# Kernel optimization log

Hardware: AMD Instinct MI355X
Metric: run time of the kernel (lower is better)

## Reference

```python
import jax, jax.numpy as jnp
import numpy as np

INF = 100000.0
B, W, T, U, S, N = 64, 16, 64, 128, 20, 8


def setup_inputs() -> dict:
    key = jax.random.key(0)
    ks = jax.random.split(key, 9)
    xavier = (2.0 / (U + U)) ** 0.5
    return {
        "slot_utt_h": jax.random.normal(ks[0], (B, W, T, U), jnp.float32),
        "slot_candidate_c": jax.random.normal(ks[1], (S, U), jnp.float32),
        "status_candidate_c": jax.random.normal(ks[2], (N, U), jnp.float32),
        "position_encoding": jax.random.normal(ks[3], (B, W, S, U), jnp.float32),
        "q_status": jax.random.normal(ks[4], (B, W, N, U), jnp.float32),
        "mask": jnp.zeros((B, W, S * N), jnp.float32),
        "weight": jax.random.normal(ks[5], (U, U), jnp.float32) * xavier,  # bilinear co-attention weight [U,U]
        "W1": jax.random.normal(ks[6], (2 * U, U), jnp.float32) * 0.05,
        "b1": jnp.zeros((U,), jnp.float32),
        "W2": jax.random.normal(ks[7], (U, U), jnp.float32) * 0.05,
        "b2": jnp.zeros((U,), jnp.float32),
        "W3": jax.random.normal(ks[8], (U, 1), jnp.float32) * 0.05,
        "b3": jnp.zeros((1,), jnp.float32),
    }


def _zero_mask(p):
    # original: -(p == 0).float() * INF, added before softmax
    return jnp.where(p == 0.0, -INF, 0.0)


def reference(slot_utt_h, slot_candidate_c, status_candidate_c, position_encoding,
              q_status, mask, weight, W1, b1, W2, b2, W3, b3):
    # ---- attention over utterance tokens ----
    # p[b,w,s,t] = <slot_candidate_c[s], slot_utt_h[b,w,t]>
    p = jnp.einsum('su,bwtu->bwst', slot_candidate_c, slot_utt_h)
    p = jax.nn.softmax(p + _zero_mask(p), axis=-1)
    q_slot = jnp.einsum('bwst,bwtu->bwsu', p, slot_utt_h) + position_encoding  # [B,W,S,U]

    # ---- bilinear co-attention: [B,W*S,U] @ weight @ [B,U,W*N] -> [B,W,S,W,N] ----
    co = jnp.einsum('bwsu,uv,bxnv->bwsxn', q_slot, weight, q_status)
    p2 = jax.nn.softmax(co + _zero_mask(co), axis=3)  # softmax over the second window axis x

    # weighted sum of statuses over window axis x
    q_status_slot = jnp.einsum('bwsxn,bxnu->bwsnu', p2, q_status)  # [B,W,S,N,U]

    q_slot_exp = jnp.broadcast_to(q_slot[:, :, :, None, :], (B, W, S, N, U))
    features = jnp.concatenate([q_slot_exp, q_status_slot], axis=-1)  # [B,W,S,N,2U]

    # ---- MLP (dropout in eval mode = identity) ----
    h = jax.nn.relu(features @ W1 + b1)
    h = jax.nn.relu(h @ W2 + b2)
    logits = h @ W3 + b3  # [B,W,S,N,1]

    logits = logits.reshape(B, W, S * N)
    slot_pred_logits = jnp.max(logits + mask, axis=1)  # masked max-pool over window
    slot_pred_labels = (slot_pred_logits > 0.0).astype(jnp.float32)
    return (slot_pred_labels, S * N, slot_pred_logits)
```

## Files before the change

### kernel.cpp

```cpp
#include <hip/hip_runtime.h>
#include <math.h>

#define INF_ 100000.0f
constexpr int B_ = 64, W_ = 16, T_ = 64, U_ = 128, S_ = 20, N_ = 8;

typedef unsigned short ushort_t;
typedef __attribute__((ext_vector_type(8))) short bf16x8;
typedef __attribute__((ext_vector_type(4))) float floatx4;

static __device__ __forceinline__ unsigned short f2bf(float x) {
    unsigned int u = __float_as_uint(x);
    return (unsigned short)((u + 0x7fff + ((u >> 16) & 1)) >> 16);
}
static __device__ __forceinline__ float bf2f(unsigned short s) {
    return __uint_as_float(((unsigned int)s) << 16);
}

__global__ __launch_bounds__(256) void k0_cast(
    const float* __restrict__ q_status, const float* __restrict__ weight,
    const float* __restrict__ W1, const float* __restrict__ W2,
    ushort_t* __restrict__ qstat_bf, ushort_t* __restrict__ wcomb,
    ushort_t* __restrict__ w1botT, ushort_t* __restrict__ w2T)
{
    int idx = blockIdx.x * 256 + threadIdx.x;
    if (idx < 1048576) { qstat_bf[idx] = f2bf(q_status[idx]); return; }
    idx -= 1048576;
    if (idx < 32768) {
        int j = idx >> 7, k = idx & 127;
        float v = (j < 128) ? weight[k * 128 + j] : W1[k * 128 + (j - 128)];
        wcomb[idx] = f2bf(v); return;
    }
    idx -= 32768;
    if (idx < 16384) {
        int j = idx >> 7, k = idx & 127;
        w1botT[idx] = f2bf(W1[(128 + k) * 128 + j]); return;
    }
    idx -= 16384;
    if (idx < 16384) {
        int j = idx >> 7, k = idx & 127;
        w2T[idx] = f2bf(W2[k * 128 + j]); return;
    }
}

__global__ __launch_bounds__(256) void k1_attn(
    const float* __restrict__ h,
    const float* __restrict__ c,
    const float* __restrict__ pos,
    ushort_t* __restrict__ q_slot_bf)
{
    __shared__ __align__(16) ushort_t sh_h[64 * 136];
    __shared__ __align__(16) ushort_t sh_hT[128 * 72];
    __shared__ __align__(16) ushort_t sh_c[32 * 136];
    __shared__ __align__(16) float    sh_sc[32 * 68];
    __shared__ __align__(16) ushort_t sh_P[32 * 72];

    const int bw = blockIdx.x, tid = threadIdx.x;
    const float* hb = h + (size_t)bw * 8192;
    for (int i = tid; i < 8192; i += 256) {
        int t = i >> 7, u = i & 127;
        ushort_t v = f2bf(hb[i]);
        sh_h[t * 136 + u] = v;
        sh_hT[u * 72 + t] = v;
    }
    for (int i = tid; i < 4096; i += 256) {
        int s = i >> 7;
        sh_c[s * 136 + (i & 127)] = (s < 20) ? f2bf(c[i]) : (ushort_t)0;
    }
    for (int i = tid; i < 32 * 72; i += 256) sh_P[i] = 0;
    __syncthreads();

    const int wave = tid >> 6, lane = tid & 63, m16 = lane & 15, q = lane >> 4;

#pragma unroll
    for (int ci = 0; ci < 2; ++ci) {
        int cmb = wave * 2 + ci;
        int mt = cmb >> 2, jt = cmb & 3;
        floatx4 acc = {0.f, 0.f, 0.f, 0.f};
#pragma unroll
        for (int kt = 0; kt < 4; ++kt) {
            bf16x8 a = *(const bf16x8*)&sh_c[(mt * 16 + m16) * 136 + kt * 32 + q * 8];
            bf16x8 b = *(const bf16x8*)&sh_h[(jt * 16 + m16) * 136 + kt * 32 + q * 8];
            acc = __builtin_amdgcn_mfma_f32_16x16x32_bf16(a, b, acc, 0, 0, 0);
        }
#pragma unroll
        for (int reg = 0; reg < 4; ++reg)
            sh_sc[(mt * 16 + q * 4 + reg) * 68 + jt * 16 + m16] = acc[reg];
    }
    __syncthreads();

    for (int s = wave; s < 20; s += 4) {
        float v = sh_sc[s * 68 + lane];
        if (v == 0.0f) v = -INF_;
        float m = v;
        for (int d = 32; d; d >>= 1) m = fmaxf(m, __shfl_xor(m, d));
        float e = expf(v - m);
        float sum = e;
        for (int d = 32; d; d >>= 1) sum += __shfl_xor(sum, d);
        sh_P[s * 72 + lane] = f2bf(e / sum);
    }
    __syncthreads();

    const size_t obase = (size_t)bw * 2560;
#pragma unroll
    for (int ci = 0; ci < 4; ++ci) {
        int cmb = wave * 4 + ci;
        int mt = cmb >> 3, jt = cmb & 7;
        floatx4 acc = {0.f, 0.f, 0.f, 0.f};
#pragma unroll
        for (int kt = 0; kt < 2; ++kt) {
            bf16x8 a = *(const bf16x8*)&sh_P[(mt * 16 + m16) * 72 + kt * 32 + q * 8];
            bf16x8 b = *(const bf16x8*)&sh_hT[(jt * 16 + m16) * 72 + kt * 32 + q * 8];
            acc = __builtin_amdgcn_mfma_f32_16x16x32_bf16(a, b, acc, 0, 0, 0);
        }
        int u = jt * 16 + m16;
#pragma unroll
        for (int reg = 0; reg < 4; ++reg) {
            int row = mt * 16 + q * 4 + reg;
            if (row < 20)
                q_slot_bf[obase + row * 128 + u] =
                    f2bf(acc[reg] + pos[obase + row * 128 + u]);
        }
    }
}

__global__ __launch_bounds__(256) void k2a(
    const ushort_t* __restrict__ qs_bf,
    const ushort_t* __restrict__ wcomb,
    const float* __restrict__ b1,
    ushort_t* __restrict__ qw_bf,
    float* __restrict__ A)
{
    __shared__ __align__(16) ushort_t sh_w[256 * 136];
    const int tid = threadIdx.x;
    for (int i = tid * 4; i < 32768; i += 1024) {
        int j = i >> 7, k = i & 127;
        *(ushort4*)&sh_w[j * 136 + k] = *(const ushort4*)&wcomb[i];
    }
    __syncthreads();

    const int wave = tid >> 6, lane = tid & 63, m16 = lane & 15, q = lane >> 4;
    const size_t row = (size_t)blockIdx.x * 64 + wave * 16 + m16;

    floatx4 acc[16];
#pragma unroll
    for (int jt = 0; jt < 16; ++jt) acc[jt] = (floatx4){0.f, 0.f, 0.f, 0.f};

#pragma unroll
    for (int kt = 0; kt < 4; ++kt) {
        bf16x8 a = *(const bf16x8*)&qs_bf[row * 128 + kt * 32 + q * 8];
#pragma unroll
        for (int jt = 0; jt < 16; ++jt) {
            bf16x8 b = *(const bf16x8*)&sh_w[(jt * 16 + m16) * 136 + kt * 32 + q * 8];
            acc[jt] = __builtin_amdgcn_mfma_f32_16x16x32_bf16(a, b, acc[jt], 0, 0, 0);
        }
    }

    const size_t orow0 = (size_t)blockIdx.x * 64 + wave * 16 + q * 4;
#pragma unroll
    for (int jt = 0; jt < 16; ++jt) {
        int col = jt * 16 + m16;
        if (col < 128) {
#pragma unroll
            for (int reg = 0; reg < 4; ++reg)
                qw_bf[(orow0 + reg) * 128 + col] = f2bf(acc[jt][reg]);
        } else {
            float bv = b1[col - 128];
#pragma unroll
            for (int reg = 0; reg < 4; ++reg)
                A[(orow0 + reg) * 128 + (col - 128)] = acc[jt][reg] + bv;
        }
    }
}

__global__ __launch_bounds__(256) void k2b(
    const ushort_t* __restrict__ qstat_bf,
    const ushort_t* __restrict__ w1botT,
    ushort_t* __restrict__ qs1_bf)
{
    __shared__ __align__(16) ushort_t sh_w[128 * 136];
    const int tid = threadIdx.x;
    for (int i = tid * 4; i < 16384; i += 1024) {
        int j = i >> 7, k = i & 127;
        *(ushort4*)&sh_w[j * 136 + k] = *(const ushort4*)&w1botT[i];
    }
    __syncthreads();

    const int wave = tid >> 6, lane = tid & 63, m16 = lane & 15, q = lane >> 4;
    const size_t row = (size_t)blockIdx.x * 64 + wave * 16 + m16;

    floatx4 acc[8];
#pragma unroll
    for (int jt = 0; jt < 8; ++jt) acc[jt] = (floatx4){0.f, 0.f, 0.f, 0.f};
#pragma unroll
    for (int kt = 0; kt < 4; ++kt) {
        bf16x8 a = *(const bf16x8*)&qstat_bf[row * 128 + kt * 32 + q * 8];
#pragma unroll
        for (int jt = 0; jt < 8; ++jt) {
            bf16x8 b = *(const bf16x8*)&sh_w[(jt * 16 + m16) * 136 + kt * 32 + q * 8];
            acc[jt] = __builtin_amdgcn_mfma_f32_16x16x32_bf16(a, b, acc[jt], 0, 0, 0);
        }
    }
    const size_t orow0 = (size_t)blockIdx.x * 64 + wave * 16 + q * 4;
#pragma unroll
    for (int jt = 0; jt < 8; ++jt) {
        int col = jt * 16 + m16;
#pragma unroll
        for (int reg = 0; reg < 4; ++reg)
            qs1_bf[(orow0 + reg) * 128 + col] = f2bf(acc[jt][reg]);
    }
}

__global__ __launch_bounds__(256) void k3_co(
    const ushort_t* __restrict__ qw_bf,
    const ushort_t* __restrict__ qstat_bf,
    float* __restrict__ co)
{
    __shared__ __align__(16) ushort_t sh_y[128 * 136];
    const int tid = threadIdx.x, rt = blockIdx.x, b = blockIdx.y;
    for (int i = tid * 4; i < 16384; i += 1024) {
        int j = i >> 7, k = i & 127;
        *(ushort4*)&sh_y[j * 136 + k] = *(const ushort4*)&qstat_bf[(size_t)b * 16384 + i];
    }
    __syncthreads();

    const int wave = tid >> 6, lane = tid & 63, m16 = lane & 15, q = lane >> 4;
    const size_t rbase = (size_t)b * 320 + rt * 64 + wave * 16;

    floatx4 acc[8];
#pragma unroll
    for (int jt = 0; jt < 8; ++jt) acc[jt] = (floatx4){0.f, 0.f, 0.f, 0.f};
#pragma unroll
    for (int kt = 0; kt < 4; ++kt) {
        bf16x8 a = *(const bf16x8*)&qw_bf[(rbase + m16) * 128 + kt * 32 + q * 8];
#pragma unroll
        for (int jt = 0; jt < 8; ++jt) {
            bf16x8 b2_ = *(const bf16x8*)&sh_y[(jt * 16 + m16) * 136 + kt * 32 + q * 8];
            acc[jt] = __builtin_amdgcn_mfma_f32_16x16x32_bf16(a, b2_, acc[jt], 0, 0, 0);
        }
    }
#pragma unroll
    for (int jt = 0; jt < 8; ++jt)
#pragma unroll
        for (int reg = 0; reg < 4; ++reg)
            co[(rbase + q * 4 + reg) * 128 + jt * 16 + m16] = acc[jt][reg];
}

__global__ __launch_bounds__(640, 3) void k4_fused(
    const float* __restrict__ co,
    const ushort_t* __restrict__ qs1_bf,
    const float* __restrict__ A,
    const ushort_t* __restrict__ w2T,
    const float* __restrict__ b2,
    const float* __restrict__ W3,
    const float* __restrict__ b3,
    float* __restrict__ lg)
{
    __shared__ __align__(16) ushort_t sh_qs1[128 * 136];
    __shared__ __align__(16) ushort_t sh_w2t[128 * 136];
    __shared__ __align__(16) float sh_p2[20 * 128];

    const int bw = blockIdx.x, b = bw >> 4, tid = threadIdx.x;

    for (int i = tid * 4; i < 16384; i += 2560) {
        int r = i >> 7, k = i & 127;
        *(ushort4*)&sh_qs1[r * 136 + k] = *(const ushort4*)&qs1_bf[(size_t)b * 16384 + i];
        *(ushort4*)&sh_w2t[r * 136 + k] = *(const ushort4*)&w2T[i];
    }

    if (tid < 160) {
        int s = tid >> 3, n = tid & 7;
        const float* crow = co + ((size_t)bw * 20 + s) * 128;
        float v[16];
        float m = -INFINITY;
#pragma unroll
        for (int x = 0; x < 16; ++x) {
            float t = crow[x * 8 + n];
            if (t == 0.0f) t = -INF_;
            v[x] = t;
            m = fmaxf(m, t);
        }
        float sum = 0.f;
#pragma unroll
        for (int x = 0; x < 16; ++x) { v[x] = expf(v[x] - m); sum += v[x]; }
        float r = 1.0f / sum;
#pragma unroll
        for (int x = 0; x < 16; ++x) sh_p2[s * 128 + x * 8 + n] = v[x] * r;
    }
    __syncthreads();

    const int wave = tid >> 6, lane = tid & 63, m16 = lane & 15, q = lane >> 4;
    const int row = wave * 16 + m16;
    const int s = row >> 3, n = row & 7;

    floatx4 acc[8];
#pragma unroll
    for (int jt = 0; jt < 8; ++jt) acc[jt] = (floatx4){0.f, 0.f, 0.f, 0.f};

    const float* Ab = A + (size_t)bw * 20 * 128;

#pragma unroll
    for (int kt = 0; kt < 4; ++kt) {
        const int k0 = kt * 32 + q * 8;
        bf16x8 bfr[8];
#pragma unroll
        for (int jt = 0; jt < 8; ++jt)
            bfr[jt] = *(const bf16x8*)&sh_w2t[(jt * 16 + m16) * 136 + k0];

        float hv[8];
        const float* ar = Ab + s * 128 + k0;
        float4 a0 = *(const float4*)ar;
        float4 a1 = *(const float4*)(ar + 4);
        hv[0] = a0.x; hv[1] = a0.y; hv[2] = a0.z; hv[3] = a0.w;
        hv[4] = a1.x; hv[5] = a1.y; hv[6] = a1.z; hv[7] = a1.w;
#pragma unroll
        for (int x = 0; x < 16; ++x) {
            float p = sh_p2[s * 128 + x * 8 + n];
            bf16x8 qv = *(const bf16x8*)&sh_qs1[(x * 8 + n) * 136 + k0];
            hv[0] += p * bf2f((ushort_t)qv[0]);
            hv[1] += p * bf2f((ushort_t)qv[1]);
            hv[2] += p * bf2f((ushort_t)qv[2]);
            hv[3] += p * bf2f((ushort_t)qv[3]);
            hv[4] += p * bf2f((ushort_t)qv[4]);
            hv[5] += p * bf2f((ushort_t)qv[5]);
            hv[6] += p * bf2f((ushort_t)qv[6]);
            hv[7] += p * bf2f((ushort_t)qv[7]);
        }
        bf16x8 af;
#pragma unroll
        for (int e = 0; e < 8; ++e) af[e] = (short)f2bf(fmaxf(hv[e], 0.f));
#pragma unroll
        for (int jt = 0; jt < 8; ++jt)
            acc[jt] = __builtin_amdgcn_mfma_f32_16x16x32_bf16(
                af, bfr[jt], acc[jt], 0, 0, 0);
    }

    float b2v[8], w3v[8];
#pragma unroll
    for (int jt = 0; jt < 8; ++jt) {
        b2v[jt] = b2[jt * 16 + m16];
        w3v[jt] = W3[jt * 16 + m16];
    }
    const float b3v = b3[0];

#pragma unroll
    for (int reg = 0; reg < 4; ++reg) {
        float p = 0.f;
#pragma unroll
        for (int jt = 0; jt < 8; ++jt)
            p += fmaxf(acc[jt][reg] + b2v[jt], 0.f) * w3v[jt];
        p += __shfl_xor(p, 1);
        p += __shfl_xor(p, 2);
        p += __shfl_xor(p, 4);
        p += __shfl_xor(p, 8);
        if (m16 == 0)
            lg[(size_t)bw * 160 + wave * 16 + q * 4 + reg] = p + b3v;
    }
}

__global__ __launch_bounds__(256) void k5_final(
    const float* __restrict__ lg,
    const float* __restrict__ mask,
    float* __restrict__ out)
{
    int idx = blockIdx.x * 256 + threadIdx.x;
    const int SN = S_ * N_;
    if (idx < B_ * SN) {
        int b = idx / SN, sn = idx % SN;
        float m = -INFINITY;
        for (int w = 0; w < W_; ++w) {
            float v = lg[((size_t)b * W_ + w) * SN + sn] + mask[((size_t)b * W_ + w) * SN + sn];
            m = fmaxf(m, v);
        }
        out[idx] = (m > 0.f) ? 1.f : 0.f;
        out[B_ * SN + 1 + idx] = m;
    }
    if (idx == 0) out[B_ * SN] = (float)SN;
}

extern "C" void kernel_launch(void* const* d_in, const int* in_sizes, int n_in,
                              void* d_out, int out_size, void* d_ws, size_t ws_size,
                              hipStream_t stream) {
    const float* slot_utt_h = (const float*)d_in[0];
    const float* slot_candidate_c = (const float*)d_in[1];
    const float* position_encoding = (const float*)d_in[3];
    const float* q_status = (const float*)d_in[4];
    const float* mask = (const float*)d_in[5];
    const float* weight = (const float*)d_in[6];
    const float* W1 = (const float*)d_in[7];
    const float* b1 = (const float*)d_in[8];
    const float* W2 = (const float*)d_in[9];
    const float* b2 = (const float*)d_in[10];
    const float* W3 = (const float*)d_in[11];
    const float* b3 = (const float*)d_in[12];
    float* out = (float*)d_out;

    float* f = (float*)d_ws;
    ushort_t* q_slot_bf = (ushort_t*)(f + 0);
    ushort_t* qw_bf     = (ushort_t*)(f + 1310720);
    float*    A         = f + 2621440;
    ushort_t* qs1_bf    = (ushort_t*)(f + 5242880);
    float*    co        = f + 5767168;
    float*    lg        = f + 8388608;
    ushort_t* qstat_bf  = (ushort_t*)(f + 8552448);
    ushort_t* wcomb     = (ushort_t*)(f + 9076736);
    ushort_t* w1botT    = (ushort_t*)(f + 9093120);
    ushort_t* w2T       = (ushort_t*)(f + 9101312);

    k0_cast<<<4352, 256, 0, stream>>>(q_status, weight, W1, W2,
                                      qstat_bf, wcomb, w1botT, w2T);
    k1_attn<<<1024, 256, 0, stream>>>(slot_utt_h, slot_candidate_c,
                                      position_encoding, q_slot_bf);
    k2b<<<128, 256, 0, stream>>>(qstat_bf, w1botT, qs1_bf);
    k2a<<<320, 256, 0, stream>>>(q_slot_bf, wcomb, b1, qw_bf, A);
    k3_co<<<dim3(5, 64), 256, 0, stream>>>(qw_bf, qstat_bf, co);
    k4_fused<<<1024, 640, 0, stream>>>(co, qs1_bf, A, w2T, b2, W3, b3, lg);
    k5_final<<<(B_ * S_ * N_ + 255) / 256, 256, 0, stream>>>(lg, mask, out);
}
```

Before: 211.5 us.

## Compute status-weighted sum in k4 via MFMA with transposed qs1 layout

The per-thread scalar FMA loop in k4 that mixed p2 weights with qs1 rows is replaced by MFMA. k2b now writes qs1 transposed per batch, and p2 is stored as bf16 in shared memory and scattered into a diagonal-masked B fragment. The ReLU'd first-layer activations are staged through shared memory before the second MFMA GEMM, and LDS use is cut so occupancy can rise (launch bounds 640,5). Separately, k2a is retiled to 512-thread blocks covering 128 rows so the weight tile is loaded half as often. The p2 weights now carry bf16 precision, and k4 gains extra synchronisation and a mostly-zero B operand.

After: 199.2 us. -5.8%, faster.

```diff
diff --git a/kernel.cpp b/kernel.cpp
--- a/kernel.cpp
+++ b/kernel.cpp
@@ -11,9 +11,6 @@
 static __device__ __forceinline__ unsigned short f2bf(float x) {
     unsigned int u = __float_as_uint(x);
     return (unsigned short)((u + 0x7fff + ((u >> 16) & 1)) >> 16);
-}
-static __device__ __forceinline__ float bf2f(unsigned short s) {
-    return __uint_as_float(((unsigned int)s) << 16);
 }
 
 __global__ __launch_bounds__(256) void k0_cast(
@@ -123,7 +120,7 @@
     }
 }
 
-__global__ __launch_bounds__(256) void k2a(
+__global__ __launch_bounds__(512, 2) void k2a(
     const ushort_t* __restrict__ qs_bf,
     const ushort_t* __restrict__ wcomb,
     const float* __restrict__ b1,
@@ -132,14 +129,14 @@
 {
     __shared__ __align__(16) ushort_t sh_w[256 * 136];
     const int tid = threadIdx.x;
-    for (int i = tid * 4; i < 32768; i += 1024) {
+    for (int i = tid * 4; i < 32768; i += 2048) {
         int j = i >> 7, k = i & 127;
         *(ushort4*)&sh_w[j * 136 + k] = *(const ushort4*)&wcomb[i];
     }
     __syncthreads();
 
     const int wave = tid >> 6, lane = tid & 63, m16 = lane & 15, q = lane >> 4;
-    const size_t row = (size_t)blockIdx.x * 64 + wave * 16 + m16;
+    const size_t row = (size_t)blockIdx.x * 128 + wave * 16 + m16;
 
     floatx4 acc[16];
 #pragma unroll
@@ -155,7 +152,7 @@
         }
     }
 
-    const size_t orow0 = (size_t)blockIdx.x * 64 + wave * 16 + q * 4;
+    const size_t orow0 = (size_t)blockIdx.x * 128 + wave * 16 + q * 4;
 #pragma unroll
     for (int jt = 0; jt < 16; ++jt) {
         int col = jt * 16 + m16;
@@ -175,7 +172,7 @@
 __global__ __launch_bounds__(256) void k2b(
     const ushort_t* __restrict__ qstat_bf,
     const ushort_t* __restrict__ w1botT,
-    ushort_t* __restrict__ qs1_bf)
+    ushort_t* __restrict__ qs1T_bf)
 {
     __shared__ __align__(16) ushort_t sh_w[128 * 136];
     const int tid = threadIdx.x;
@@ -205,8 +202,11 @@
     for (int jt = 0; jt < 8; ++jt) {
         int col = jt * 16 + m16;
 #pragma unroll
-        for (int reg = 0; reg < 4; ++reg)
-            qs1_bf[(orow0 + reg) * 128 + col] = f2bf(acc[jt][reg]);
+        for (int reg = 0; reg < 4; ++reg) {
+            size_t grow = orow0 + reg;
+            qs1T_bf[(grow >> 7) * 16384 + (size_t)col * 128 + (grow & 127)]
+                = f2bf(acc[jt][reg]);
+        }
     }
 }
 
@@ -245,9 +245,9 @@
             co[(rbase + q * 4 + reg) * 128 + jt * 16 + m16] = acc[jt][reg];
 }
 
-__global__ __launch_bounds__(640, 3) void k4_fused(
+__global__ __launch_bounds__(640, 5) void k4_fused(
     const float* __restrict__ co,
-    const ushort_t* __restrict__ qs1_bf,
+    const ushort_t* __restrict__ qs1T_bf,
     const float* __restrict__ A,
     const ushort_t* __restrict__ w2T,
     const float* __restrict__ b2,
@@ -255,16 +255,15 @@
     const float* __restrict__ b3,
     float* __restrict__ lg)
 {
-    __shared__ __align__(16) ushort_t sh_qs1[128 * 136];
     __shared__ __align__(16) ushort_t sh_w2t[128 * 136];
-    __shared__ __align__(16) float sh_p2[20 * 128];
+    __shared__ __align__(16) ushort_t sh_u[160 * 136];
 
     const int bw = blockIdx.x, b = bw >> 4, tid = threadIdx.x;
 
     for (int i = tid * 4; i < 16384; i += 2560) {
         int r = i >> 7, k = i & 127;
-        *(ushort4*)&sh_qs1[r * 136 + k] = *(const ushort4*)&qs1_bf[(size_t)b * 16384 + i];
         *(ushort4*)&sh_w2t[r * 136 + k] = *(const ushort4*)&w2T[i];
+        *(ushort4*)&sh_u[r * 136 + k] = *(const ushort4*)&qs1T_bf[(size_t)b * 16384 + i];
     }
 
     if (tid < 160) {
@@ -284,54 +283,69 @@
         for (int x = 0; x < 16; ++x) { v[x] = expf(v[x] - m); sum += v[x]; }
         float r = 1.0f / sum;
 #pragma unroll
-        for (int x = 0; x < 16; ++x) sh_p2[s * 128 + x * 8 + n] = v[x] * r;
+        for (int x = 0; x < 16; ++x)
+            sh_u[17408 + s * 132 + x * 8 + n] = f2bf(v[x] * r);
     }
     __syncthreads();
 
     const int wave = tid >> 6, lane = tid & 63, m16 = lane & 15, q = lane >> 4;
-    const int row = wave * 16 + m16;
-    const int s = row >> 3, n = row & 7;
+    const int n = m16 & 7;
+    const int sIdx = wave * 2 + (m16 >> 3);
+    const int rowS = wave * 16 + m16;
+
+    floatx4 gacc[8];
+#pragma unroll
+    for (int mt = 0; mt < 8; ++mt) gacc[mt] = (floatx4){0.f, 0.f, 0.f, 0.f};
+
+#pragma unroll
+    for (int kt = 0; kt < 4; ++kt) {
+        short pv = (short)sh_u[17408 + sIdx * 132 + kt * 32 + q * 8 + n];
+        bf16x8 pf = {0, 0, 0, 0, 0, 0, 0, 0};
+        pf[0] = (n == 0) ? pv : (short)0;
+        pf[1] = (n == 1) ? pv : (short)0;
+        pf[2] = (n == 2) ? pv : (short)0;
+        pf[3] = (n == 3) ? pv : (short)0;
+        pf[4] = (n == 4) ? pv : (short)0;
+        pf[5] = (n == 5) ? pv : (short)0;
+        pf[6] = (n == 6) ? pv : (short)0;
+        pf[7] = (n == 7) ? pv : (short)0;
+#pragma unroll
+        for (int mt = 0; mt < 8; ++mt) {
+            bf16x8 af = *(const bf16x8*)&sh_u[(mt * 16 + m16) * 136 + kt * 32 + q * 8];
+            gacc[mt] = __builtin_amdgcn_mfma_f32_16x16x32_bf16(af, pf, gacc[mt], 0, 0, 0);
+        }
+    }
+    __syncthreads();
+
+    {
+        const float* Ab = A + ((size_t)bw * 20 + sIdx) * 128;
+#pragma unroll
+        for (int mt = 0; mt < 8; ++mt) {
+            int u0 = mt * 16 + q * 4;
+            float4 av = *(const float4*)&Ab[u0];
+            ushort4 o;
+            o.x = f2bf(fmaxf(gacc[mt][0] + av.x, 0.f));
+            o.y = f2bf(fmaxf(gacc[mt][1] + av.y, 0.f));
+            o.z = f2bf(fmaxf(gacc[mt][2] + av.z, 0.f));
+            o.w = f2bf(fmaxf(gacc[mt][3] + av.w, 0.f));
+            *(ushort4*)&sh_u[rowS * 136 + u0] = o;
+        }
+    }
+    __syncthreads();
 
     floatx4 acc[8];
 #pragma unroll
     for (int jt = 0; jt < 8; ++jt) acc[jt] = (floatx4){0.f, 0.f, 0.f, 0.f};
-
-    const float* Ab = A + (size_t)bw * 20 * 128;
 
 #pragma unroll
     for (int kt = 0; kt < 4; ++kt) {
         const int k0 = kt * 32 + q * 8;
-        bf16x8 bfr[8];
-#pragma unroll
-        for (int jt = 0; jt < 8; ++jt)
-            bfr[jt] = *(const bf16x8*)&sh_w2t[(jt * 16 + m16) * 136 + k0];
-
-        float hv[8];
-        const float* ar = Ab + s * 128 + k0;
-        float4 a0 = *(const float4*)ar;
-        float4 a1 = *(const float4*)(ar + 4);
-        hv[0] = a0.x; hv[1] = a0.y; hv[2] = a0.z; hv[3] = a0.w;
-        hv[4] = a1.x; hv[5] = a1.y; hv[6] = a1.z; hv[7] = a1.w;
-#pragma unroll
-        for (int x = 0; x < 16; ++x) {
-            float p = sh_p2[s * 128 + x * 8 + n];
-            bf16x8 qv = *(const bf16x8*)&sh_qs1[(x * 8 + n) * 136 + k0];
-            hv[0] += p * bf2f((ushort_t)qv[0]);
-            hv[1] += p * bf2f((ushort_t)qv[1]);
-            hv[2] += p * bf2f((ushort_t)qv[2]);
-            hv[3] += p * bf2f((ushort_t)qv[3]);
-            hv[4] += p * bf2f((ushort_t)qv[4]);
-            hv[5] += p * bf2f((ushort_t)qv[5]);
-            hv[6] += p * bf2f((ushort_t)qv[6]);
-            hv[7] += p * bf2f((ushort_t)qv[7]);
-        }
-        bf16x8 af;
-#pragma unroll
-        for (int e = 0; e < 8; ++e) af[e] = (short)f2bf(fmaxf(hv[e], 0.f));
-#pragma unroll
-        for (int jt = 0; jt < 8; ++jt)
-            acc[jt] = __builtin_amdgcn_mfma_f32_16x16x32_bf16(
-                af, bfr[jt], acc[jt], 0, 0, 0);
+        bf16x8 af = *(const bf16x8*)&sh_u[rowS * 136 + k0];
+#pragma unroll
+        for (int jt = 0; jt < 8; ++jt) {
+            bf16x8 bfr = *(const bf16x8*)&sh_w2t[(jt * 16 + m16) * 136 + k0];
+            acc[jt] = __builtin_amdgcn_mfma_f32_16x16x32_bf16(af, bfr, acc[jt], 0, 0, 0);
+        }
     }
 
     float b2v[8], w3v[8];
@@ -398,7 +412,7 @@
     ushort_t* q_slot_bf = (ushort_t*)(f + 0);
     ushort_t* qw_bf     = (ushort_t*)(f + 1310720);
     float*    A         = f + 2621440;
-    ushort_t* qs1_bf    = (ushort_t*)(f + 5242880);
+    ushort_t* qs1T_bf   = (ushort_t*)(f + 5242880);
     float*    co        = f + 5767168;
     float*    lg        = f + 8388608;
     ushort_t* qstat_bf  = (ushort_t*)(f + 8552448);
@@ -410,9 +424,9 @@
                                       qstat_bf, wcomb, w1botT, w2T);
     k1_attn<<<1024, 256, 0, stream>>>(slot_utt_h, slot_candidate_c,
                                       position_encoding, q_slot_bf);
-    k2b<<<128, 256, 0, stream>>>(qstat_bf, w1botT, qs1_bf);
-    k2a<<<320, 256, 0, stream>>>(q_slot_bf, wcomb, b1, qw_bf, A);
+    k2b<<<128, 256, 0, stream>>>(qstat_bf, w1botT, qs1T_bf);
+    k2a<<<160, 512, 0, stream>>>(q_slot_bf, wcomb, b1, qw_bf, A);
     k3_co<<<dim3(5, 64), 256, 0, stream>>>(qw_bf, qstat_bf, co);
-    k4_fused<<<1024, 640, 0, stream>>>(co, qs1_bf, A, w2T, b2, W3, b3, lg);
+    k4_fused<<<1024, 640, 0, stream>>>(co, qs1T_bf, A, w2T, b2, W3, b3, lg);
     k5_final<<<(B_ * S_ * N_ + 255) / 256, 256, 0, stream>>>(lg, mask, out);
 }
```
